# Optimization experiments

Measured on AMD Instinct MI355X. Metric: run time of the kernel, lower is better.

The kernel has to match this reference:

```python
import jax, jax.numpy as jnp
import numpy as np

B, T, E, H, OUT, L = 128, 512, 256, 512, 9, 2


def setup_inputs() -> dict:
    key = jax.random.key(0)
    ks = jax.random.split(key, 6)
    def lin(k, shape, fan_in):
        return (jax.random.normal(k, shape, jnp.float32) / np.float32(np.sqrt(fan_in)))
    return {
        "embeddings": jax.random.normal(ks[0], (B, T, E), jnp.float32),
        "W_w": lin(ks[1], (H, E), E),
        "W_b": jnp.zeros((H,), jnp.float32),
        "Uk_w": lin(ks[2], (L, H, H), H),
        "Uk_b": jnp.zeros((L, H), jnp.float32),
        "Wk_w": lin(ks[3], (L - 1, H, H), H),
        "Wk_b": jnp.zeros((L - 1, H), jnp.float32),
        "V_w": lin(ks[4], (OUT, H), H),
        "V_b": jnp.zeros((OUT,), jnp.float32),
    }


def reference(embeddings, W_w, W_b, Uk_w, Uk_b, Wk_w, Wk_b, V_w, V_b):
    n_layers = Uk_w.shape[0]
    bsz = embeddings.shape[0]
    hid = W_w.shape[0]
    # Input projection W(x_t) is time-independent: do it once as a big GEMM. [B,T,H]
    xproj = jnp.einsum('bte,he->bth', embeddings, W_w) + W_b

    def step(z_prev, xp_t):
        # z_prev: [L, B, H]; xp_t: [B, H]
        z = jnp.tanh(xp_t + z_prev[0] @ Uk_w[0].T + Uk_b[0])
        zs = [z]
        for l in range(n_layers - 1):
            # NOTE: original code uses Uks[l] (not Uks[l+1]) here -- reproduced faithfully.
            z = jnp.tanh(z @ Wk_w[l].T + Wk_b[l] + z_prev[l + 1] @ Uk_w[l].T + Uk_b[l])
            zs.append(z)
        y = z @ V_w.T + V_b  # [B, OUT]
        return jnp.stack(zs, 0), y

    z0 = jnp.zeros((n_layers, bsz, hid), embeddings.dtype)
    _, ys = jax.lax.scan(step, z0, jnp.swapaxes(xproj, 0, 1))  # ys: [T, B, OUT]
    return jnp.swapaxes(ys, 0, 1)  # [B, T, OUT]
```

## Files before the change

### kernel.cpp

```cpp
#include <hip/hip_runtime.h>
#include <hip/hip_fp16.h>

typedef _Float16 half8 __attribute__((ext_vector_type(8)));
typedef float floatx4 __attribute__((ext_vector_type(4)));
typedef unsigned int u32x4 __attribute__((ext_vector_type(4)));


union H8 { half8 v; unsigned long long u[2]; };

__device__ __forceinline__ bool valid16(unsigned long long u) {
  return (unsigned)((unsigned)(u & 0xFFFFull) - 0x3C00u) <= 0x600u;
}

__device__ __forceinline__ void poll16(const unsigned long long* src, int tid,
                                       unsigned long long g[8], unsigned need, int sleep) {
  while (need) {
    u32x4 r[4];
#pragma unroll
    for (int j = 0; j < 4; ++j)
      if (need & (3u << (2 * j))) {
        const char* p = (const char*)(src + 2 * (tid + j * 256));
        asm volatile("global_load_dwordx4 %0, %1, off sc0 sc1"
                     : "=&v"(r[j]) : "v"(p) : "memory");
      }
    asm volatile("s_waitcnt vmcnt(0)" ::: "memory");
    __builtin_amdgcn_sched_barrier(0);
    unsigned nn = 0;
#pragma unroll
    for (int j = 0; j < 4; ++j) {
      if (!(need & (3u << (2 * j)))) continue;
      unsigned long long lo = ((unsigned long long)r[j][1] << 32) | r[j][0];
      unsigned long long hi = ((unsigned long long)r[j][3] << 32) | r[j][2];
      if (need & (1u << (2 * j))) { if (valid16(lo)) g[2 * j] = lo; else nn |= (1u << (2 * j)); }
      if (need & (2u << (2 * j))) { if (valid16(hi)) g[2 * j + 1] = hi; else nn |= (2u << (2 * j)); }
    }
    need = nn;
    if (need && sleep) __builtin_amdgcn_s_sleep(1);
  }
}

__global__ void prep_small(const float* __restrict__ Vw, const float* __restrict__ Vb,
                           const float* __restrict__ Wb, const float* __restrict__ Ukb,
                           const float* __restrict__ Wkb, const float* __restrict__ Ukw,
                           const float* __restrict__ Wkw, _Float16* __restrict__ V16,
                           float* __restrict__ bxp, float* __restrict__ bc,
                           float* __restrict__ sums) {
  int i = blockIdx.x * blockDim.x + threadIdx.x;
  if (i < 16 * 512) {
    int o = i >> 9, k = i & 511;
    V16[i] = (_Float16)(o < 9 ? Vw[o * 512 + k] : 0.0f);
  }
  if (i < 512) {
    bxp[i] = Wb[i] + Ukb[i];
    bc[i]  = Wkb[i] + Ukb[i];
  }
  if (i < 1024) {
    const float* row = (i < 512) ? Ukw + (size_t)i * 512 : Wkw + (size_t)(i - 512) * 512;
    float s = 0.f;
    for (int k = 0; k < 512; k += 4) {
      float4 v = *(const float4*)(row + k);
      s += (float)(_Float16)v.x + (float)(_Float16)v.y + (float)(_Float16)v.z + (float)(_Float16)v.w;
    }
    sums[i] = s;
  } else if (i < 1040) {
    int o = i - 1024;
    float s = 0.f;
    if (o < 9) {
      const float* row = Vw + (size_t)o * 512;
      for (int k = 0; k < 512; k += 4) {
        float4 v = *(const float4*)(row + k);
        s += (float)(_Float16)v.x + (float)(_Float16)v.y + (float)(_Float16)v.z + (float)(_Float16)v.w;
      }
    }
    sums[i] = (o < 9 ? Vb[o] : 0.f) - 2.f * s;
  }
}

__global__ __launch_bounds__(256) void gemm_xp(const float* __restrict__ Aptr,
                                               const float* __restrict__ Bptr,
                                               _Float16* __restrict__ Cout,
                                               const float* __restrict__ bias) {
  const int K = 256;
  __shared__ __align__(16) _Float16 As[128][40];
  __shared__ __align__(16) _Float16 Bs[128][40];
  const int tid = threadIdx.x;
  const int bm = blockIdx.x, bn = blockIdx.y;
  const int w = tid >> 6, lane = tid & 63;
  const int m = lane & 15, q = lane >> 4;

  floatx4 acc[2][8];
#pragma unroll
  for (int i = 0; i < 2; ++i)
#pragma unroll
    for (int j = 0; j < 8; ++j) acc[i][j] = (floatx4){0.f, 0.f, 0.f, 0.f};

  for (int kt = 0; kt < (K >> 5); ++kt) {
    const int k0 = kt << 5;
    __syncthreads();
#pragma unroll
    for (int it = 0; it < 2; ++it) {
      int idx = tid + it * 256;
      int row = idx >> 2, ch = idx & 3;
      size_t gA = (size_t)(bm * 128 + row) * K + (k0 + ch * 8);
      const float4* p = (const float4*)(Aptr + gA);
      float4 f0 = p[0], f1 = p[1];
      *(half8*)&As[row][ch * 8] =
          (half8){(_Float16)f0.x, (_Float16)f0.y, (_Float16)f0.z, (_Float16)f0.w,
                  (_Float16)f1.x, (_Float16)f1.y, (_Float16)f1.z, (_Float16)f1.w};
      size_t gB = (size_t)(bn * 128 + row) * K + (k0 + ch * 8);
      const float4* pb = (const float4*)(Bptr + gB);
      float4 g0 = pb[0], g1 = pb[1];
      *(half8*)&Bs[row][ch * 8] =
          (half8){(_Float16)g0.x, (_Float16)g0.y, (_Float16)g0.z, (_Float16)g0.w,
                  (_Float16)g1.x, (_Float16)g1.y, (_Float16)g1.z, (_Float16)g1.w};
    }
    __syncthreads();
    half8 a[2], b[8];
#pragma unroll
    for (int i = 0; i < 2; ++i) a[i] = *(const half8*)&As[w * 32 + i * 16 + m][q * 8];
#pragma unroll
    for (int j = 0; j < 8; ++j) b[j] = *(const half8*)&Bs[j * 16 + m][q * 8];
#pragma unroll
    for (int i = 0; i < 2; ++i)
#pragma unroll
      for (int j = 0; j < 8; ++j)
        acc[i][j] = __builtin_amdgcn_mfma_f32_16x16x32_f16(a[i], b[j], acc[i][j], 0, 0, 0);
  }
#pragma unroll
  for (int i = 0; i < 2; ++i)
#pragma unroll
    for (int j = 0; j < 8; ++j) {
      int col = bn * 128 + j * 16 + m;
      float bv = bias[col];
#pragma unroll
      for (int rr = 0; rr < 4; ++rr) {
        int row = bm * 128 + w * 32 + i * 16 + q * 4 + rr;
        size_t orow = (size_t)(row & 511) * 128 + (row >> 9);
        Cout[orow * 512 + col] = (_Float16)(acc[i][j][rr] + bv);
      }
    }
}

template <int SLEEP>
__device__ __forceinline__ void stage_tile(const _Float16* srcTile, _Float16* dst, int tid) {
  const unsigned long long* src = (const unsigned long long*)srcTile;
  u32x4 r[4];
#pragma unroll
  for (int j = 0; j < 4; ++j) {
    const char* p = (const char*)(src + 2 * (tid + j * 256));
    asm volatile("global_load_dwordx4 %0, %1, off sc0 sc1" : "=&v"(r[j]) : "v"(p) : "memory");
  }
  asm volatile("s_waitcnt vmcnt(0)" ::: "memory");
  __builtin_amdgcn_sched_barrier(0);
  unsigned long long g[8];
  unsigned need = 0;
#pragma unroll
  for (int j = 0; j < 4; ++j) {
    unsigned long long lo = ((unsigned long long)r[j][1] << 32) | r[j][0];
    unsigned long long hi = ((unsigned long long)r[j][3] << 32) | r[j][2];
    if (valid16(lo)) g[2 * j] = lo; else need |= (1u << (2 * j));
    if (valid16(hi)) g[2 * j + 1] = hi; else need |= (2u << (2 * j));
  }
  poll16(src, tid, g, need, SLEEP);
#pragma unroll
  for (int j = 0; j < 4; ++j) {
    H8 t;
    t.u[0] = g[2 * j];
    t.u[1] = g[2 * j + 1];
    *(half8*)&dst[(tid + j * 256) * 8] = t.v;
  }
}

__global__ __launch_bounds__(256, 1) void rnn_fused2(const float* __restrict__ Uw,
                                                     const float* __restrict__ Wkw,
                                                     const _Float16* __restrict__ xp,
                                                     _Float16* __restrict__ z0f,
                                                     _Float16* __restrict__ z1f,
                                                     const float* __restrict__ bc,
                                                     const float* __restrict__ sums) {
  __shared__ __align__(16) _Float16 az[2][8192];
  __shared__ __align__(16) _Float16 azs[8192];
  __shared__ __align__(16) _Float16 zo[4][16][40];
  const int tid = threadIdx.x;
  const int layer = blockIdx.x >> 5, bt = blockIdx.x & 7, ct = (blockIdx.x >> 3) & 3;
  const int lane = tid & 63, w = tid >> 6, m = lane & 15, q = lane >> 4;
  const int colbase = ct * 128 + w * 32;
  const int cs = ct * 4 + w;

  half8 ufr[2][16], wfr[2][16];
#pragma unroll
  for (int t = 0; t < 2; ++t) {
    const float* up = Uw + (size_t)(colbase + t * 16 + m) * 512 + q * 8;
    const float* wp = Wkw + (size_t)(colbase + t * 16 + m) * 512 + q * 8;
#pragma unroll
    for (int kk = 0; kk < 16; ++kk) {
      float4 f0 = *(const float4*)(up + kk * 32), f1 = *(const float4*)(up + kk * 32 + 4);
      ufr[t][kk] = (half8){(_Float16)f0.x, (_Float16)f0.y, (_Float16)f0.z, (_Float16)f0.w,
                           (_Float16)f1.x, (_Float16)f1.y, (_Float16)f1.z, (_Float16)f1.w};
      if (layer) {
        float4 g0 = *(const float4*)(wp + kk * 32), g1 = *(const float4*)(wp + kk * 32 + 4);
        wfr[t][kk] = (half8){(_Float16)g0.x, (_Float16)g0.y, (_Float16)g0.z, (_Float16)g0.w,
                             (_Float16)g1.x, (_Float16)g1.y, (_Float16)g1.z, (_Float16)g1.w};
      }
    }
  }
  const float corrU[2] = {-2.f * sums[colbase + m], -2.f * sums[colbase + 16 + m]};
  float cw[2] = {0.f, 0.f};
  if (layer) {
    cw[0] = -2.f * sums[512 + colbase + m] + bc[colbase + m];
    cw[1] = -2.f * sums[512 + colbase + 16 + m] + bc[colbase + 16 + m];
  }

  _Float16* zout = layer ? z1f : z0f;

  if (layer) stage_tile<1>(z0f + (size_t)bt * 8192, azs, tid);

  for (int s = 0; s < 512; ++s) {
    float pin[8];
    if (layer == 0) {
      const _Float16* xb = xp + (size_t)s * 65536 + (size_t)(bt * 16) * 512;
#pragma unroll
      for (int t = 0; t < 2; ++t)
#pragma unroll
        for (int rr = 0; rr < 4; ++rr)
          pin[t * 4 + rr] = (float)xb[(size_t)(q * 4 + rr) * 512 + colbase + t * 16 + m];
    }

    floatx4 wk[2];
    wk[0] = (floatx4){0.f, 0.f, 0.f, 0.f};
    wk[1] = (floatx4){0.f, 0.f, 0.f, 0.f};
    _Float16* azcur = layer ? az[0] : az[s & 1];
    if (layer) {
      __syncthreads();
      const unsigned long long* src =
          (const unsigned long long*)(z1f + ((size_t)(s - 1) * 8 + bt) * 8192);
      u32x4 r16[4];
      if (s > 0) {
#pragma unroll
        for (int j = 0; j < 4; ++j) {
          const char* p = (const char*)(src + 2 * (tid + j * 256));
          asm volatile("global_load_dwordx4 %0, %1, off sc0 sc1"
                       : "=&v"(r16[j]) : "v"(p) : "memory");
        }
      }
#pragma unroll
      for (int kk = 0; kk < 16; ++kk) {
        half8 a = *(const half8*)&azs[((kk * 4 + q) * 16 + m) * 8];
        wk[0] = __builtin_amdgcn_mfma_f32_16x16x32_f16(a, wfr[0][kk], wk[0], 0, 0, 0);
        wk[1] = __builtin_amdgcn_mfma_f32_16x16x32_f16(a, wfr[1][kk], wk[1], 0, 0, 0);
      }
      if (s > 0) {
        asm volatile("s_waitcnt vmcnt(0)" ::: "memory");
        __builtin_amdgcn_sched_barrier(0);
        unsigned long long g[8];
        unsigned need = 0;
#pragma unroll
        for (int j = 0; j < 4; ++j) {
          unsigned long long lo = ((unsigned long long)r16[j][1] << 32) | r16[j][0];
          unsigned long long hi = ((unsigned long long)r16[j][3] << 32) | r16[j][2];
          if (valid16(lo)) g[2 * j] = lo; else need |= (1u << (2 * j));
          if (valid16(hi)) g[2 * j + 1] = hi; else need |= (2u << (2 * j));
        }
        poll16(src, tid, g, need, 0);
#pragma unroll
        for (int j = 0; j < 4; ++j) {
          H8 t;
          t.u[0] = g[2 * j];
          t.u[1] = g[2 * j + 1];
          *(half8*)&azcur[(tid + j * 256) * 8] = t.v;
        }
      }
    } else {
      if (s > 0) stage_tile<0>(z0f + ((size_t)(s - 1) * 8 + bt) * 8192, azcur, tid);
    }
    __syncthreads();

    floatx4 acc[2][2];
    acc[0][0] = (floatx4){0.f, 0.f, 0.f, 0.f};
    acc[0][1] = (floatx4){0.f, 0.f, 0.f, 0.f};
    acc[1][0] = (floatx4){0.f, 0.f, 0.f, 0.f};
    acc[1][1] = (floatx4){0.f, 0.f, 0.f, 0.f};
    if (s > 0) {
#pragma unroll
      for (int kk = 0; kk < 16; ++kk) {
        half8 a = *(const half8*)&azcur[((kk * 4 + q) * 16 + m) * 8];
        acc[0][kk & 1] = __builtin_amdgcn_mfma_f32_16x16x32_f16(a, ufr[0][kk], acc[0][kk & 1], 0, 0, 0);
        acc[1][kk & 1] = __builtin_amdgcn_mfma_f32_16x16x32_f16(a, ufr[1][kk], acc[1][kk & 1], 0, 0, 0);
      }
    }
#pragma unroll
    for (int t = 0; t < 2; ++t)
#pragma unroll
      for (int rr = 0; rr < 4; ++rr) {
        float x = layer ? (wk[t][rr] + cw[t]) : pin[t * 4 + rr];
        if (s > 0) x += acc[t][0][rr] + acc[t][1][rr] + corrU[t];
        float e = __builtin_exp2f(x * 2.885390081777927f);
        float enc = 3.f - 2.f * __builtin_amdgcn_rcpf(e + 1.f);
        zo[w][q * 4 + rr][t * 16 + m] = (_Float16)enc;
      }
    asm volatile("s_waitcnt lgkmcnt(0)" ::: "memory");
    __builtin_amdgcn_sched_barrier(0);
    {
      H8 pv;
      pv.v = *(const half8*)&zo[w][m][q * 8];
      unsigned long long* dst =
          (unsigned long long*)((char*)zout +
                                (((size_t)s * 8 + bt) * 1024 + (size_t)(cs * 4 + q) * 16 + m) * 16);
      u32x4 pd;
      pd[0] = (unsigned)pv.u[0];
      pd[1] = (unsigned)(pv.u[0] >> 32);
      pd[2] = (unsigned)pv.u[1];
      pd[3] = (unsigned)(pv.u[1] >> 32);
      asm volatile("global_store_dwordx4 %0, %1, off sc0 sc1" :: "v"(dst), "v"(pd) : "memory");
    }
    if (layer && s < 511)
      stage_tile<1>(z0f + ((size_t)(s + 1) * 8 + bt) * 8192, azs, tid);
  }
}

__global__ __launch_bounds__(64) void out_gemm(const _Float16* __restrict__ z1,
                                               const _Float16* __restrict__ V16,
                                               const float* __restrict__ bco,
                                               float* __restrict__ out) {
  __shared__ __align__(16) _Float16 zt[16][520];
  __shared__ __align__(16) _Float16 vt[16][520];
  const int tid = threadIdx.x;
  const int m = tid & 15, q = tid >> 4;
  const size_t r0 = (size_t)blockIdx.x * 16;
  for (int idx = tid; idx < 1024; idx += 64) {
    int row = idx >> 6, ch = idx & 63;
    int r = (int)(r0 + row), t = r >> 7, b = r & 127;
    size_t off = (size_t)(t * 8 + (b >> 4)) * 8192 + (size_t)ch * 128 + (b & 15) * 8;
    *(half8*)&zt[row][ch * 8] = *(const half8*)&z1[off];
    *(half8*)&vt[row][ch * 8] = *(const half8*)&V16[(size_t)row * 512 + ch * 8];
  }
  __syncthreads();
  floatx4 acc = {0.f, 0.f, 0.f, 0.f};
#pragma unroll
  for (int kk = 0; kk < 16; ++kk) {
    half8 a = *(const half8*)&zt[m][kk * 32 + q * 8];
    half8 b = *(const half8*)&vt[m][kk * 32 + q * 8];
    acc = __builtin_amdgcn_mfma_f32_16x16x32_f16(a, b, acc, 0, 0, 0);
  }
  if (m < 9) {
#pragma unroll
    for (int rr = 0; rr < 4; ++rr) {
      size_t r = r0 + q * 4 + rr;
      size_t t = r >> 7, b = r & 127;
      out[(b * 512 + t) * 9 + m] = acc[rr] + bco[m];
    }
  }
}

extern "C" void kernel_launch(void* const* d_in, const int* in_sizes, int n_in,
                              void* d_out, int out_size, void* d_ws, size_t ws_size,
                              hipStream_t stream) {
  const float* emb = (const float*)d_in[0];
  const float* Ww  = (const float*)d_in[1];
  const float* Wb  = (const float*)d_in[2];
  const float* Ukw = (const float*)d_in[3];
  const float* Ukb = (const float*)d_in[4];
  const float* Wkw = (const float*)d_in[5];
  const float* Wkb = (const float*)d_in[6];
  const float* Vw  = (const float*)d_in[7];
  const float* Vb  = (const float*)d_in[8];
  float* out = (float*)d_out;

  char* ws = (char*)d_ws;
  _Float16* xp   = (_Float16*)(ws + 0);
  _Float16* z0f  = (_Float16*)(ws + 67108864);
  _Float16* z1f  = (_Float16*)(ws + 134217728);
  _Float16* V16  = (_Float16*)(ws + 201326592);
  float* bxp     = (float*)(ws + 201342976);
  float* bc      = (float*)(ws + 201345024);
  float* sums    = (float*)(ws + 201347072);

  hipLaunchKernelGGL(prep_small, dim3(32), dim3(256), 0, stream,
                     Vw, Vb, Wb, Ukb, Wkb, Ukw, Wkw, V16, bxp, bc, sums);
  hipLaunchKernelGGL(gemm_xp, dim3(512, 4), dim3(256), 0, stream, emb, Ww, xp, bxp);
  hipLaunchKernelGGL(rnn_fused2, dim3(64), dim3(256), 0, stream,
                     Ukw, Wkw, xp, z0f, z1f, bc, sums);
  hipLaunchKernelGGL(out_gemm, dim3(4096), dim3(64), 0, stream, z1f, V16, sums + 1024, out);
}
```

Before: 1.623 ms.

## Halve recurrent column tiles per block and keep own hidden slice in LDS

The persistent RNN kernel now runs 32 blocks of 512 threads, so each block owns 256 hidden columns instead of 128. Each step it writes its own output slice straight into LDS and polls global memory only for the other block's half, rather than re-reading the whole 8192-element state tile. This is meant to cut cross-block polling traffic and the number of blocks that have to synchronise through global memory. In exchange each block carries twice the waves and register pressure, and the launch bounds of two blocks per CU may force register spills.

```diff
diff --git a/kernel.cpp b/kernel.cpp
--- a/kernel.cpp
+++ b/kernel.cpp
@@ -12,31 +12,64 @@
   return (unsigned)((unsigned)(u & 0xFFFFull) - 0x3C00u) <= 0x600u;
 }
 
-__device__ __forceinline__ void poll16(const unsigned long long* src, int tid,
-                                       unsigned long long g[8], unsigned need, int sleep) {
+__device__ __forceinline__ unsigned val16B(u32x4 r, unsigned long long g[2]) {
+  unsigned long long lo = ((unsigned long long)r[1] << 32) | r[0];
+  unsigned long long hi = ((unsigned long long)r[3] << 32) | r[2];
+  unsigned need = 0;
+  if (valid16(lo)) g[0] = lo; else need |= 1u;
+  if (valid16(hi)) g[1] = hi; else need |= 2u;
+  return need;
+}
+
+__device__ __forceinline__ void retry16B(const char* addr, unsigned long long g[2],
+                                         unsigned need, int sleep) {
   while (need) {
-    u32x4 r[4];
-#pragma unroll
-    for (int j = 0; j < 4; ++j)
-      if (need & (3u << (2 * j))) {
-        const char* p = (const char*)(src + 2 * (tid + j * 256));
-        asm volatile("global_load_dwordx4 %0, %1, off sc0 sc1"
-                     : "=&v"(r[j]) : "v"(p) : "memory");
-      }
+    if (sleep) __builtin_amdgcn_s_sleep(1);
+    u32x4 r;
+    asm volatile("global_load_dwordx4 %0, %1, off sc0 sc1" : "=&v"(r) : "v"(addr) : "memory");
     asm volatile("s_waitcnt vmcnt(0)" ::: "memory");
     __builtin_amdgcn_sched_barrier(0);
-    unsigned nn = 0;
-#pragma unroll
-    for (int j = 0; j < 4; ++j) {
-      if (!(need & (3u << (2 * j)))) continue;
-      unsigned long long lo = ((unsigned long long)r[j][1] << 32) | r[j][0];
-      unsigned long long hi = ((unsigned long long)r[j][3] << 32) | r[j][2];
-      if (need & (1u << (2 * j))) { if (valid16(lo)) g[2 * j] = lo; else nn |= (1u << (2 * j)); }
-      if (need & (2u << (2 * j))) { if (valid16(hi)) g[2 * j + 1] = hi; else nn |= (2u << (2 * j)); }
-    }
-    need = nn;
-    if (need && sleep) __builtin_amdgcn_s_sleep(1);
-  }
+    unsigned long long lo = ((unsigned long long)r[1] << 32) | r[0];
+    unsigned long long hi = ((unsigned long long)r[3] << 32) | r[2];
+    if ((need & 1u) && valid16(lo)) { g[0] = lo; need &= ~1u; }
+    if ((need & 2u) && valid16(hi)) { g[1] = hi; need &= ~2u; }
+  }
+}
+
+__device__ __forceinline__ void stage_azs(const _Float16* srcTile, _Float16* dst, int tid) {
+  const char* b0 = (const char*)srcTile + (size_t)tid * 16;
+  const char* b1 = (const char*)srcTile + (size_t)(tid + 512) * 16;
+  u32x4 r0, r1;
+  asm volatile("global_load_dwordx4 %0, %1, off sc0 sc1" : "=&v"(r0) : "v"(b0) : "memory");
+  asm volatile("global_load_dwordx4 %0, %1, off sc0 sc1" : "=&v"(r1) : "v"(b1) : "memory");
+  asm volatile("s_waitcnt vmcnt(0)" ::: "memory");
+  __builtin_amdgcn_sched_barrier(0);
+  unsigned long long g0[2], g1[2];
+  unsigned n0 = val16B(r0, g0), n1 = val16B(r1, g1);
+  while (n0 | n1) {
+    __builtin_amdgcn_s_sleep(1);
+    u32x4 s0, s1;
+    if (n0) asm volatile("global_load_dwordx4 %0, %1, off sc0 sc1" : "=&v"(s0) : "v"(b0) : "memory");
+    if (n1) asm volatile("global_load_dwordx4 %0, %1, off sc0 sc1" : "=&v"(s1) : "v"(b1) : "memory");
+    asm volatile("s_waitcnt vmcnt(0)" ::: "memory");
+    __builtin_amdgcn_sched_barrier(0);
+    if (n0) {
+      unsigned long long lo = ((unsigned long long)s0[1] << 32) | s0[0];
+      unsigned long long hi = ((unsigned long long)s0[3] << 32) | s0[2];
+      if ((n0 & 1u) && valid16(lo)) { g0[0] = lo; n0 &= ~1u; }
+      if ((n0 & 2u) && valid16(hi)) { g0[1] = hi; n0 &= ~2u; }
+    }
+    if (n1) {
+      unsigned long long lo = ((unsigned long long)s1[1] << 32) | s1[0];
+      unsigned long long hi = ((unsigned long long)s1[3] << 32) | s1[2];
+      if ((n1 & 1u) && valid16(lo)) { g1[0] = lo; n1 &= ~1u; }
+      if ((n1 & 2u) && valid16(hi)) { g1[1] = hi; n1 &= ~2u; }
+    }
+  }
+  H8 t0; t0.u[0] = g0[0]; t0.u[1] = g0[1];
+  *(half8*)&dst[(size_t)tid * 8] = t0.v;
+  H8 t1; t1.u[0] = g1[0]; t1.u[1] = g1[1];
+  *(half8*)&dst[(size_t)(tid + 512) * 8] = t1.v;
 }
 
 __global__ void prep_small(const float* __restrict__ Vw, const float* __restrict__ Vb,
@@ -141,37 +174,7 @@
     }
 }
 
-template <int SLEEP>
-__device__ __forceinline__ void stage_tile(const _Float16* srcTile, _Float16* dst, int tid) {
-  const unsigned long long* src = (const unsigned long long*)srcTile;
-  u32x4 r[4];
-#pragma unroll
-  for (int j = 0; j < 4; ++j) {
-    const char* p = (const char*)(src + 2 * (tid + j * 256));
-    asm volatile("global_load_dwordx4 %0, %1, off sc0 sc1" : "=&v"(r[j]) : "v"(p) : "memory");
-  }
-  asm volatile("s_waitcnt vmcnt(0)" ::: "memory");
-  __builtin_amdgcn_sched_barrier(0);
-  unsigned long long g[8];
-  unsigned need = 0;
-#pragma unroll
-  for (int j = 0; j < 4; ++j) {
-    unsigned long long lo = ((unsigned long long)r[j][1] << 32) | r[j][0];
-    unsigned long long hi = ((unsigned long long)r[j][3] << 32) | r[j][2];
-    if (valid16(lo)) g[2 * j] = lo; else need |= (1u << (2 * j));
-    if (valid16(hi)) g[2 * j + 1] = hi; else need |= (2u << (2 * j));
-  }
-  poll16(src, tid, g, need, SLEEP);
-#pragma unroll
-  for (int j = 0; j < 4; ++j) {
-    H8 t;
-    t.u[0] = g[2 * j];
-    t.u[1] = g[2 * j + 1];
-    *(half8*)&dst[(tid + j * 256) * 8] = t.v;
-  }
-}
-
-__global__ __launch_bounds__(256, 1) void rnn_fused2(const float* __restrict__ Uw,
+__global__ __launch_bounds__(512, 2) void rnn_fused2(const float* __restrict__ Uw,
                                                      const float* __restrict__ Wkw,
                                                      const _Float16* __restrict__ xp,
                                                      _Float16* __restrict__ z0f,
@@ -180,12 +183,13 @@
                                                      const float* __restrict__ sums) {
   __shared__ __align__(16) _Float16 az[2][8192];
   __shared__ __align__(16) _Float16 azs[8192];
-  __shared__ __align__(16) _Float16 zo[4][16][40];
+  __shared__ __align__(16) _Float16 zo[8][16][40];
   const int tid = threadIdx.x;
-  const int layer = blockIdx.x >> 5, bt = blockIdx.x & 7, ct = (blockIdx.x >> 3) & 3;
+  const int layer = blockIdx.x >> 4, ct = (blockIdx.x >> 3) & 1, bt = blockIdx.x & 7;
   const int lane = tid & 63, w = tid >> 6, m = lane & 15, q = lane >> 4;
-  const int colbase = ct * 128 + w * 32;
-  const int cs = ct * 4 + w;
+  const int colbase = ct * 256 + w * 32;
+  const int gSelf = ct * 512 + tid;
+  const int gPoll = (1 - ct) * 512 + tid;
 
   half8 ufr[2][16], wfr[2][16];
 #pragma unroll
@@ -212,8 +216,11 @@
   }
 
   _Float16* zout = layer ? z1f : z0f;
-
-  if (layer) stage_tile<1>(z0f + (size_t)bt * 8192, azs, tid);
+  const char* selfB = (const char*)zout;
+
+  if (layer) stage_azs(z0f + (size_t)bt * 8192, azs, tid);
+
+  H8 pvkeep;
 
   for (int s = 0; s < 512; ++s) {
     float pin[8];
@@ -232,16 +239,12 @@
     _Float16* azcur = layer ? az[0] : az[s & 1];
     if (layer) {
       __syncthreads();
-      const unsigned long long* src =
-          (const unsigned long long*)(z1f + ((size_t)(s - 1) * 8 + bt) * 8192);
-      u32x4 r16[4];
+      const char* srcB = (const char*)z1f + ((size_t)(s - 1) * 8 + bt) * 16384;
+      u32x4 r16;
       if (s > 0) {
-#pragma unroll
-        for (int j = 0; j < 4; ++j) {
-          const char* p = (const char*)(src + 2 * (tid + j * 256));
-          asm volatile("global_load_dwordx4 %0, %1, off sc0 sc1"
-                       : "=&v"(r16[j]) : "v"(p) : "memory");
-        }
+        *(half8*)&azcur[(size_t)gSelf * 8] = pvkeep.v;
+        asm volatile("global_load_dwordx4 %0, %1, off sc0 sc1"
+                     : "=&v"(r16) : "v"(srcB + (size_t)gPoll * 16) : "memory");
       }
 #pragma unroll
       for (int kk = 0; kk < 16; ++kk) {
@@ -252,26 +255,30 @@
       if (s > 0) {
         asm volatile("s_waitcnt vmcnt(0)" ::: "memory");
         __builtin_amdgcn_sched_barrier(0);
-        unsigned long long g[8];
-        unsigned need = 0;
-#pragma unroll
-        for (int j = 0; j < 4; ++j) {
-          unsigned long long lo = ((unsigned long long)r16[j][1] << 32) | r16[j][0];
-          unsigned long long hi = ((unsigned long long)r16[j][3] << 32) | r16[j][2];
-          if (valid16(lo)) g[2 * j] = lo; else need |= (1u << (2 * j));
-          if (valid16(hi)) g[2 * j + 1] = hi; else need |= (2u << (2 * j));
-        }
-        poll16(src, tid, g, need, 0);
-#pragma unroll
-        for (int j = 0; j < 4; ++j) {
-          H8 t;
-          t.u[0] = g[2 * j];
-          t.u[1] = g[2 * j + 1];
-          *(half8*)&azcur[(tid + j * 256) * 8] = t.v;
-        }
+        unsigned long long g[2];
+        unsigned need = val16B(r16, g);
+        retry16B(srcB + (size_t)gPoll * 16, g, need, 0);
+        H8 t;
+        t.u[0] = g[0];
+        t.u[1] = g[1];
+        *(half8*)&azcur[(size_t)gPoll * 8] = t.v;
       }
     } else {
-      if (s > 0) stage_tile<0>(z0f + ((size_t)(s - 1) * 8 + bt) * 8192, azcur, tid);
+      if (s > 0) {
+        const char* srcB = selfB + ((size_t)(s - 1) * 8 + bt) * 16384;
+        u32x4 r16;
+        asm volatile("global_load_dwordx4 %0, %1, off sc0 sc1"
+                     : "=&v"(r16) : "v"(srcB + (size_t)gPoll * 16) : "memory");
+        asm volatile("s_waitcnt vmcnt(0)" ::: "memory");
+        __builtin_amdgcn_sched_barrier(0);
+        unsigned long long g[2];
+        unsigned need = val16B(r16, g);
+        retry16B(srcB + (size_t)gPoll * 16, g, need, 0);
+        H8 t;
+        t.u[0] = g[0];
+        t.u[1] = g[1];
+        *(half8*)&azcur[(size_t)gPoll * 8] = t.v;
+      }
     }
     __syncthreads();
 
@@ -303,18 +310,21 @@
     {
       H8 pv;
       pv.v = *(const half8*)&zo[w][m][q * 8];
-      unsigned long long* dst =
-          (unsigned long long*)((char*)zout +
-                                (((size_t)s * 8 + bt) * 1024 + (size_t)(cs * 4 + q) * 16 + m) * 16);
+      char* dstB = (char*)zout + (((size_t)s * 8 + bt) * 1024 + (size_t)gSelf) * 16;
       u32x4 pd;
       pd[0] = (unsigned)pv.u[0];
       pd[1] = (unsigned)(pv.u[0] >> 32);
       pd[2] = (unsigned)pv.u[1];
       pd[3] = (unsigned)(pv.u[1] >> 32);
-      asm volatile("global_store_dwordx4 %0, %1, off sc0 sc1" :: "v"(dst), "v"(pd) : "memory");
+      asm volatile("global_store_dwordx4 %0, %1, off sc0 sc1" :: "v"(dstB), "v"(pd) : "memory");
+      if (layer == 0) {
+        *(half8*)&az[(s + 1) & 1][(size_t)gSelf * 8] = pv.v;
+      } else {
+        pvkeep = pv;
+      }
     }
     if (layer && s < 511)
-      stage_tile<1>(z0f + ((size_t)(s + 1) * 8 + bt) * 8192, azs, tid);
+      stage_azs(z0f + ((size_t)(s + 1) * 8 + bt) * 8192, azs, tid);
   }
 }
 
@@ -378,7 +388,7 @@
   hipLaunchKernelGGL(prep_small, dim3(32), dim3(256), 0, stream,
                      Vw, Vb, Wb, Ukb, Wkb, Ukw, Wkw, V16, bxp, bc, sums);
   hipLaunchKernelGGL(gemm_xp, dim3(512, 4), dim3(256), 0, stream, emb, Ww, xp, bxp);
-  hipLaunchKernelGGL(rnn_fused2, dim3(64), dim3(256), 0, stream,
+  hipLaunchKernelGGL(rnn_fused2, dim3(32), dim3(512), 0, stream,
                      Ukw, Wkw, xp, z0f, z1f, bc, sums);
   hipLaunchKernelGGL(out_gemm, dim3(4096), dim3(64), 0, stream, z1f, V16, sums + 1024, out);
 }
```

New measurement: 3.624 ms. +123.3%, slower.
